# Performance work log

Hardware: AMD Instinct MI355X
Metric: run time of the kernel (lower is better)

Reference implementation:

```python
import jax, jax.numpy as jnp
import numpy as np

N_TOK, BATCH, D, MEM, H, W = 196, 64, 256, 2048, 16, 16


def setup_inputs() -> dict:
    key = jax.random.key(0)
    ks = jax.random.split(key, 9)
    w_scale = 1.0 / np.sqrt(D)  # ~ Linear default init scale
    return {
        "input_tokens": jax.random.normal(ks[0], (N_TOK, BATCH, D), jnp.float32),
        "ch_memory": jax.random.normal(ks[1], (MEM, D), jnp.float32) * 0.1,
        "ch_wq": jax.random.normal(ks[2], (D, D), jnp.float32) * w_scale,
        "ch_wk": jax.random.normal(ks[3], (D, D), jnp.float32) * w_scale,
        "ch_wv": jax.random.normal(ks[4], (D, D), jnp.float32) * w_scale,
        "sp_memory": jax.random.normal(ks[5], (MEM, H, W), jnp.float32) * 0.1,
        "sp_wq": jax.random.normal(ks[6], (D, D), jnp.float32) * w_scale,
        "sp_wk": jax.random.normal(ks[7], (D, D), jnp.float32) * w_scale,
        "sp_wv": jax.random.normal(ks[8], (D, D), jnp.float32) * w_scale,
    }


def reference(input_tokens, ch_memory, ch_wq, ch_wk, ch_wv,
              sp_memory, sp_wq, sp_wk, sp_wv):
    n_tok, batch, d = input_tokens.shape
    hw = d  # spatial branch requires feature_dim == H*W
    x = input_tokens.reshape(n_tok * batch, d)  # [NB, D]

    # ---- Channel memory branch: dot-product softmax read ----
    q = x @ ch_wq.T                       # [NB, D]
    k = ch_memory @ ch_wk.T               # [M, D]
    v = ch_memory @ ch_wv.T               # [M, D]
    scores = (q @ k.T) * (1.0 / jnp.sqrt(jnp.float32(d)))  # [NB, M]
    att_c = jax.nn.softmax(scores, axis=-1)
    out_c = att_c @ v                     # [NB, D]

    # ---- Spatial memory branch: SSIM-score softmax read ----
    mem_flat = sp_memory.reshape(sp_memory.shape[0], hw)  # [M, HW]
    qf = x @ sp_wq.T                      # [NB, HW]
    kf = mem_flat @ sp_wk.T               # [M, HW]
    vf = mem_flat @ sp_wv.T               # [M, HW]

    q_mean = jnp.mean(qf, axis=1, keepdims=True)          # [NB, 1]
    k_mean = jnp.mean(kf, axis=1, keepdims=True)          # [M, 1]
    q_var = jnp.var(qf, axis=1, ddof=1, keepdims=True)    # unbiased, like torch.var
    k_var = jnp.var(kf, axis=1, ddof=1, keepdims=True)
    cov = ((qf - q_mean) @ (kf - k_mean).T) / jnp.float32(hw - 1)  # [NB, M]

    c1, c2 = 0.01, 0.03
    mean_prod = q_mean @ k_mean.T                          # [NB, M]
    numerator = (2.0 * mean_prod + c1) * (2.0 * cov + c2)
    denominator = (q_mean ** 2 + (k_mean.T) ** 2 + c1) * (q_var + k_var.T + c2)
    ssim = numerator / (denominator + 1e-8)                # [NB, M]

    att_s = jax.nn.softmax(ssim, axis=-1)
    out_s = att_s @ vf                     # [NB, HW] == [NB, D]

    return (out_c + out_s).reshape(n_tok, batch, d)
```

## Files before the change

### kernel.cpp

```cpp
#include <hip/hip_runtime.h>

#define NBQ 12544
#define DM  256
#define MM  2048

typedef __attribute__((ext_vector_type(8)))  __bf16 bf16x8;
typedef __attribute__((ext_vector_type(4)))  float  floatx4;

__device__ __forceinline__ ushort f2bf(float x) {
    unsigned u = __float_as_uint(x);
    u += 0x7fffu + ((u >> 16) & 1u);
    return (ushort)(u >> 16);
}
__device__ __forceinline__ float bf2f(ushort h) {
    return __uint_as_float(((unsigned)h) << 16);
}

__device__ __forceinline__ void glds16(const ushort* g, ushort* l) {
    __builtin_amdgcn_global_load_lds(
        (const __attribute__((address_space(1))) unsigned int*)g,
        (__attribute__((address_space(3))) unsigned int*)l, 16, 0, 0);
}

__global__ __launch_bounds__(256) void gemm_proj_all(
    const float* __restrict__ x,      const float* __restrict__ ch_mem,
    const float* __restrict__ ch_wq,  const float* __restrict__ ch_wk,
    const float* __restrict__ ch_wv,  const float* __restrict__ sp_mem,
    const float* __restrict__ sp_wq,  const float* __restrict__ sp_wk,
    const float* __restrict__ sp_wv,
    ushort* __restrict__ Qb,  ushort* __restrict__ QFb,
    ushort* __restrict__ Kb,  ushort* __restrict__ KFb,
    ushort* __restrict__ Vtb, ushort* __restrict__ VFtb)
{
    __shared__ ushort As[64][72];
    __shared__ ushort W1s[64][72];
    __shared__ ushort W2s[64][72];

    int bid = blockIdx.x;
    const float* A; const float* W1; const float* W2;
    ushort* C1; ushort* C2; int nrows, trans2;
    if (bid < 784) {
        A = x; W1 = ch_wq; W2 = sp_wq; C1 = Qb; C2 = QFb; nrows = NBQ; trans2 = 0;
    } else if (bid < 912) {
        A = ch_mem; W1 = ch_wk; W2 = ch_wv; C1 = Kb; C2 = Vtb;
        nrows = MM; trans2 = 1; bid -= 784;
    } else {
        A = sp_mem; W1 = sp_wk; W2 = sp_wv; C1 = KFb; C2 = VFtb;
        nrows = MM; trans2 = 1; bid -= 912;
    }
    const int r0 = (bid >> 2) * 64;
    const int c0 = (bid & 3) * 64;

    const int tid  = threadIdx.x;
    const int wv   = tid >> 6;
    const int lane = tid & 63;
    const int quad = lane >> 4;
    const int l16  = lane & 15;
    const int rw = (wv & 1) * 32;
    const int cw = (wv >> 1) * 32;

    floatx4 acc1[2][2], acc2[2][2];
    #pragma unroll
    for (int i = 0; i < 2; ++i)
        #pragma unroll
        for (int j = 0; j < 2; ++j) {
            acc1[i][j] = (floatx4){0.f, 0.f, 0.f, 0.f};
            acc2[i][j] = (floatx4){0.f, 0.f, 0.f, 0.f};
        }

    for (int d0 = 0; d0 < 256; d0 += 64) {
        __syncthreads();
        #pragma unroll
        for (int it = 0; it < 4; ++it) {
            int idx = tid + it * 256;
            int r = idx >> 4, c4 = (idx & 15) * 4;
            float4 a4 = *(const float4*)(A  + (size_t)(r0 + r) * 256 + d0 + c4);
            float4 w14 = *(const float4*)(W1 + (size_t)(c0 + r) * 256 + d0 + c4);
            float4 w24 = *(const float4*)(W2 + (size_t)(c0 + r) * 256 + d0 + c4);
            ushort4 ab, w1b, w2b;
            ab.x = f2bf(a4.x);  ab.y = f2bf(a4.y);  ab.z = f2bf(a4.z);  ab.w = f2bf(a4.w);
            w1b.x = f2bf(w14.x); w1b.y = f2bf(w14.y); w1b.z = f2bf(w14.z); w1b.w = f2bf(w14.w);
            w2b.x = f2bf(w24.x); w2b.y = f2bf(w24.y); w2b.z = f2bf(w24.z); w2b.w = f2bf(w24.w);
            *(ushort4*)&As[r][c4]  = ab;
            *(ushort4*)&W1s[r][c4] = w1b;
            *(ushort4*)&W2s[r][c4] = w2b;
        }
        __syncthreads();
        #pragma unroll
        for (int kk = 0; kk < 64; kk += 32) {
            bf16x8 aA0 = *(const bf16x8*)&As[rw + l16][kk + quad * 8];
            bf16x8 aA1 = *(const bf16x8*)&As[rw + 16 + l16][kk + quad * 8];
            bf16x8 b10 = *(const bf16x8*)&W1s[cw + l16][kk + quad * 8];
            bf16x8 b11 = *(const bf16x8*)&W1s[cw + 16 + l16][kk + quad * 8];
            bf16x8 b20 = *(const bf16x8*)&W2s[cw + l16][kk + quad * 8];
            bf16x8 b21 = *(const bf16x8*)&W2s[cw + 16 + l16][kk + quad * 8];
            acc1[0][0] = __builtin_amdgcn_mfma_f32_16x16x32_bf16(aA0, b10, acc1[0][0], 0, 0, 0);
            acc1[0][1] = __builtin_amdgcn_mfma_f32_16x16x32_bf16(aA0, b11, acc1[0][1], 0, 0, 0);
            acc1[1][0] = __builtin_amdgcn_mfma_f32_16x16x32_bf16(aA1, b10, acc1[1][0], 0, 0, 0);
            acc1[1][1] = __builtin_amdgcn_mfma_f32_16x16x32_bf16(aA1, b11, acc1[1][1], 0, 0, 0);
            acc2[0][0] = __builtin_amdgcn_mfma_f32_16x16x32_bf16(aA0, b20, acc2[0][0], 0, 0, 0);
            acc2[0][1] = __builtin_amdgcn_mfma_f32_16x16x32_bf16(aA0, b21, acc2[0][1], 0, 0, 0);
            acc2[1][0] = __builtin_amdgcn_mfma_f32_16x16x32_bf16(aA1, b20, acc2[1][0], 0, 0, 0);
            acc2[1][1] = __builtin_amdgcn_mfma_f32_16x16x32_bf16(aA1, b21, acc2[1][1], 0, 0, 0);
        }
    }

    #pragma unroll
    for (int ag = 0; ag < 2; ++ag)
        #pragma unroll
        for (int cg = 0; cg < 2; ++cg)
            #pragma unroll
            for (int i = 0; i < 4; ++i)
                C1[(size_t)(r0 + rw + ag * 16 + quad * 4 + i) * 256
                   + c0 + cw + cg * 16 + l16] = f2bf(acc1[ag][cg][i]);

    if (!trans2) {
        #pragma unroll
        for (int ag = 0; ag < 2; ++ag)
            #pragma unroll
            for (int cg = 0; cg < 2; ++cg)
                #pragma unroll
                for (int i = 0; i < 4; ++i)
                    C2[(size_t)(r0 + rw + ag * 16 + quad * 4 + i) * 256
                       + c0 + cw + cg * 16 + l16] = f2bf(acc2[ag][cg][i]);
    } else {
        __syncthreads();
        #pragma unroll
        for (int ag = 0; ag < 2; ++ag)
            #pragma unroll
            for (int cg = 0; cg < 2; ++cg)
                #pragma unroll
                for (int i = 0; i < 4; ++i)
                    W2s[cw + cg * 16 + l16][rw + ag * 16 + quad * 4 + i] = f2bf(acc2[ag][cg][i]);
        __syncthreads();
        const int col = tid >> 2;
        const int seg = (tid & 3) * 16;
        #pragma unroll
        for (int j = 0; j < 2; ++j)
            *(uint4*)(C2 + (size_t)(c0 + col) * nrows + r0 + seg + j * 8) =
                *(const uint4*)&W2s[col][seg + j * 8];
    }
}

__global__ __launch_bounds__(256) void row_stats_kf(
    const ushort* __restrict__ KFb, float* __restrict__ km, float* __restrict__ kv)
{
    const int row  = blockIdx.x * 4 + (threadIdx.x >> 6);
    const int lane = threadIdx.x & 63;
    ushort4 u = *(const ushort4*)(KFb + (size_t)row * 256 + lane * 4);
    float a = bf2f(u.x), b = bf2f(u.y), c = bf2f(u.z), d = bf2f(u.w);
    float s  = a + b + c + d;
    float ss = a * a + b * b + c * c + d * d;
    #pragma unroll
    for (int off = 32; off > 0; off >>= 1) {
        s  += __shfl_down(s, off);
        ss += __shfl_down(ss, off);
    }
    if (lane == 0) {
        float m = s * (1.f / 256.f);
        km[row] = m;
        kv[row] = (ss - 256.f * m * m) * (1.f / 255.f);
    }
}

template<int NHALF>
__global__ __launch_bounds__(256, 2) void fused_attn_st(
    const ushort* __restrict__ Qb,  const ushort* __restrict__ QFb,
    const ushort* __restrict__ Kb,  const ushort* __restrict__ KFb,
    const ushort* __restrict__ Vtb, const ushort* __restrict__ VFtb,
    const float* __restrict__ km_, const float* __restrict__ kv_,
    float* __restrict__ out, float* __restrict__ part, float* __restrict__ denp)
{
    __shared__ ushort SMu[32768];
    float* combuf = (float*)SMu;

    const int tid  = threadIdx.x;
    const int wv   = tid >> 6;
    const int lane = tid & 63;
    const int quad = lane >> 4;
    const int l16  = lane & 15;
    const int qsel = wv & 1;
    const int br   = wv >> 1;

    const int bid   = blockIdx.x;
    const int half  = (NHALF == 2) ? (bid & 1) : 0;
    const int qc    = (NHALF == 2) ? (bid >> 1) : bid;
    const int q0    = qc * 32;
    const int kbase = half * (MM / NHALF);
    const int NT    = (MM / NHALF) / 32;

    const ushort* qsrc = br ? QFb : Qb;
    bf16x8 aQ[8];
    {
        const ushort* qp = qsrc + (size_t)(q0 + qsel * 16 + l16) * DM + quad * 8;
        #pragma unroll
        for (int s = 0; s < 8; ++s) aQ[s] = *(const bf16x8*)(qp + s * 32);
    }

    float qmv = 0.f, qvv = 0.f;
    if (br) {
        float sum = 0.f, ss = 0.f;
        #pragma unroll
        for (int s = 0; s < 8; ++s)
            #pragma unroll
            for (int j = 0; j < 8; ++j) {
                float v = (float)aQ[s][j];
                sum += v; ss += v * v;
            }
        sum += __shfl_xor(sum, 16, 64); sum += __shfl_xor(sum, 32, 64);
        ss  += __shfl_xor(ss, 16, 64);  ss  += __shfl_xor(ss, 32, 64);
        qmv = sum * (1.f / 256.f);
        qvv = (ss - 256.f * qmv * qmv) * (1.f / 255.f);
    }

    int offK[4], offV[4];
    #pragma unroll
    for (int p = 0; p < 4; ++p) {
        int j  = wv * 4 + p;
        int Rk = 2 * j + (lane >> 5);
        int rk = (Rk & 3) + ((Rk >> 4) & 1) * 4 + ((Rk >> 2) & 3) * 8;
        int ck = (lane & 31) ^ (Rk & 7);
        offK[p] = rk * DM + ck * 8;
        int Rv = 16 * j + (lane >> 2);
        int cv = (lane & 3) ^ (Rv & 3);
        offV[p] = Rv * MM + cv * 8;
    }

    const ushort* kp  = Kb   + (size_t)kbase * DM;
    const ushort* kfp = KFb  + (size_t)kbase * DM;
    const ushort* vp  = Vtb  + kbase;
    const ushort* vfp = VFtb + kbase;

    floatx4 acc[16];
    #pragma unroll
    for (int t = 0; t < 16; ++t) acc[t] = (floatx4){0.f, 0.f, 0.f, 0.f};
    float den = 0.f;

    const int ksw  = l16 & 7;
    const int vswo = (quad ^ (l16 & 3)) * 8;

    for (int ti = 0; ti < NT; ++ti) {
        __syncthreads();
        #pragma unroll
        for (int p = 0; p < 4; ++p) {
            int db = (wv * 4 + p) * 512;
            glds16(kp  + offK[p], SMu + db);
            glds16(kfp + offK[p], SMu + 8192 + db);
            glds16(vp  + offV[p], SMu + 16384 + db);
            glds16(vfp + offV[p], SMu + 24576 + db);
        }
        kp += 32 * DM; kfp += 32 * DM; vp += 32; vfp += 32;
        __syncthreads();

        const ushort* Ks = SMu + (br ? 8192 : 0);
        floatx4 S0 = (floatx4){0.f, 0.f, 0.f, 0.f};
        floatx4 S1 = (floatx4){0.f, 0.f, 0.f, 0.f};
        #pragma unroll
        for (int s = 0; s < 8; ++s) {
            int off = (((s * 4 + quad) ^ ksw)) * 8;
            bf16x8 aK0 = *(const bf16x8*)(Ks + l16 * DM + off);
            bf16x8 aK1 = *(const bf16x8*)(Ks + 4096 + l16 * DM + off);
            S0 = __builtin_amdgcn_mfma_f32_16x16x32_bf16(aK0, aQ[s], S0, 0, 0, 0);
            S1 = __builtin_amdgcn_mfma_f32_16x16x32_bf16(aK1, aQ[s], S1, 0, 0, 0);
        }

        const int kk = kbase + ti * 32;
        float pb[8];
        if (!br) {
            #pragma unroll
            for (int r = 0; r < 4; ++r) {
                pb[r]     = __expf(S0[r] * 0.0625f);
                pb[4 + r] = __expf(S1[r] * 0.0625f);
            }
        } else {
            floatx4 km0 = *(const floatx4*)(km_ + kk + 8 * quad);
            floatx4 km1 = *(const floatx4*)(km_ + kk + 8 * quad + 4);
            floatx4 kv0 = *(const floatx4*)(kv_ + kk + 8 * quad);
            floatx4 kv1 = *(const floatx4*)(kv_ + kk + 8 * quad + 4);
            #pragma unroll
            for (int r = 0; r < 4; ++r) {
                {
                    float mp  = qmv * km0[r];
                    float cov = (S0[r] - 256.f * mp) * (1.f / 255.f);
                    float num = (2.f * mp + 0.01f) * (2.f * cov + 0.03f);
                    float dn  = (qmv * qmv + km0[r] * km0[r] + 0.01f) * (qvv + kv0[r] + 0.03f);
                    pb[r] = __expf(num / (dn + 1e-8f));
                }
                {
                    float mp  = qmv * km1[r];
                    float cov = (S1[r] - 256.f * mp) * (1.f / 255.f);
                    float num = (2.f * mp + 0.01f) * (2.f * cov + 0.03f);
                    float dn  = (qmv * qmv + km1[r] * km1[r] + 0.01f) * (qvv + kv1[r] + 0.03f);
                    pb[4 + r] = __expf(num / (dn + 1e-8f));
                }
            }
        }
        union { ushort u[8]; bf16x8 v; } ap;
        #pragma unroll
        for (int j = 0; j < 8; ++j) {
            den += pb[j];
            ap.u[j] = f2bf(pb[j]);
        }

        const ushort* Vs = SMu + (br ? 24576 : 16384);
        #pragma unroll
        for (int t = 0; t < 16; ++t) {
            bf16x8 bV = *(const bf16x8*)(Vs + (t * 16 + l16) * 32 + vswo);
            acc[t] = __builtin_amdgcn_mfma_f32_16x16x32_bf16(ap.v, bV, acc[t], 0, 0, 0);
        }
    }

    den += __shfl_xor(den, 16, 64);
    den += __shfl_xor(den, 32, 64);

    if (NHALF == 1) {
        float rdn[4];
        #pragma unroll
        for (int r = 0; r < 4; ++r)
            rdn[r] = 1.f / __shfl(den, quad * 4 + r, 64);

        __syncthreads();
        if (br) {
            #pragma unroll
            for (int t = 0; t < 16; ++t)
                #pragma unroll
                for (int r = 0; r < 4; ++r)
                    combuf[(qsel * 16 + quad * 4 + r) * 256 + t * 16 + l16] = acc[t][r] * rdn[r];
        }
        __syncthreads();
        if (!br) {
            #pragma unroll
            for (int t = 0; t < 16; ++t)
                #pragma unroll
                for (int r = 0; r < 4; ++r) {
                    int ql = qsel * 16 + quad * 4 + r;
                    out[(size_t)(q0 + ql) * DM + t * 16 + l16] =
                        acc[t][r] * rdn[r] + combuf[ql * 256 + t * 16 + l16];
                }
        }
    } else {
        float* Np = part + (size_t)(half * 2 + br) * ((size_t)NBQ * DM);
        #pragma unroll
        for (int t = 0; t < 16; ++t)
            #pragma unroll
            for (int r = 0; r < 4; ++r)
                Np[(size_t)(q0 + qsel * 16 + quad * 4 + r) * DM + t * 16 + l16] = acc[t][r];
        if (lane < 16)
            denp[(size_t)(half * 2 + br) * NBQ + q0 + qsel * 16 + lane] = den;
    }
}

__global__ __launch_bounds__(256) void combine_halves(
    const float* __restrict__ part, const float* __restrict__ denp,
    float* __restrict__ out)
{
    const size_t stride = (size_t)NBQ * 64;
    const float4* p4 = (const float4*)part;
    float4* o4 = (float4*)out;
    #pragma unroll
    for (int u = 0; u < 2; ++u) {
        size_t i = (size_t)blockIdx.x * 512 + (size_t)u * 256 + threadIdx.x;
        int q = (int)(i >> 6);
        float rc = 1.f / (denp[q] + denp[2 * NBQ + q]);
        float rs = 1.f / (denp[NBQ + q] + denp[3 * NBQ + q]);
        float4 c0 = p4[i];
        float4 s0 = p4[stride + i];
        float4 c1 = p4[2 * stride + i];
        float4 s1 = p4[3 * stride + i];
        float4 r;
        r.x = (c0.x + c1.x) * rc + (s0.x + s1.x) * rs;
        r.y = (c0.y + c1.y) * rc + (s0.y + s1.y) * rs;
        r.z = (c0.z + c1.z) * rc + (s0.z + s1.z) * rs;
        r.w = (c0.w + c1.w) * rc + (s0.w + s1.w) * rs;
        o4[i] = r;
    }
}

extern "C" void kernel_launch(void* const* d_in, const int* in_sizes, int n_in,
                              void* d_out, int out_size, void* d_ws, size_t ws_size,
                              hipStream_t stream)
{
    const float* x      = (const float*)d_in[0];
    const float* ch_mem = (const float*)d_in[1];
    const float* ch_wq  = (const float*)d_in[2];
    const float* ch_wk  = (const float*)d_in[3];
    const float* ch_wv  = (const float*)d_in[4];
    const float* sp_mem = (const float*)d_in[5];
    const float* sp_wq  = (const float*)d_in[6];
    const float* sp_wk  = (const float*)d_in[7];
    const float* sp_wv  = (const float*)d_in[8];
    float* out = (float*)d_out;

    ushort* Qb   = (ushort*)d_ws;
    ushort* QFb  = Qb   + (size_t)NBQ * DM;
    ushort* Kb   = QFb  + (size_t)NBQ * DM;
    ushort* KFb  = Kb   + (size_t)MM * DM;
    ushort* Vtb  = KFb  + (size_t)MM * DM;
    ushort* VFtb = Vtb  + (size_t)MM * DM;
    float*  km   = (float*)(VFtb + (size_t)MM * DM);
    float*  kv   = km + MM;
    float*  part = kv + MM;
    float*  denp = part + (size_t)4 * NBQ * DM;

    const size_t base_b = (2 * (size_t)NBQ * DM + 4 * (size_t)MM * DM) * sizeof(ushort)
                        + 2 * (size_t)MM * sizeof(float);
    const size_t need   = base_b + ((size_t)4 * NBQ * DM + 4 * NBQ) * sizeof(float);
    const bool split = ws_size >= need;

    dim3 blk(256);
    gemm_proj_all<<<dim3(1040), blk, 0, stream>>>(
        x, ch_mem, ch_wq, ch_wk, ch_wv, sp_mem, sp_wq, sp_wk, sp_wv,
        Qb, QFb, Kb, KFb, Vtb, VFtb);
    row_stats_kf<<<dim3(MM / 4), blk, 0, stream>>>(KFb, km, kv);
    if (split) {
        fused_attn_st<2><<<dim3(2 * NBQ / 32), blk, 0, stream>>>(
            Qb, QFb, Kb, KFb, Vtb, VFtb, km, kv, out, part, denp);
        combine_halves<<<dim3(NBQ * DM / 4 / 512), blk, 0, stream>>>(part, denp, out);
    } else {
        fused_attn_st<1><<<dim3(NBQ / 32), blk, 0, stream>>>(
            Qb, QFb, Kb, KFb, Vtb, VFtb, km, kv, out, part, denp);
    }
}
```

Measured before the change: 287.9 us.

## Read K/V tiles directly from global memory instead of staging through LDS

The attention kernel stops cooperatively staging K, KF, V and VF tiles into shared memory with global_load_lds and barriers. Each wave now loads its MFMA operands straight from global memory (relying on L1/L2 caching), and LDS shrinks to the combine buffer. With less LDS in use, the launch bound is raised to three blocks per SM. This removes the two barriers per tile and the LDS traffic, but it risks uncoalesced, redundant global loads and exposed load latency without explicit prefetching.

After: 603.7 us. 110% more time.

```diff
diff --git a/kernel.cpp b/kernel.cpp
--- a/kernel.cpp
+++ b/kernel.cpp
@@ -14,12 +14,6 @@
 }
 __device__ __forceinline__ float bf2f(ushort h) {
     return __uint_as_float(((unsigned)h) << 16);
-}
-
-__device__ __forceinline__ void glds16(const ushort* g, ushort* l) {
-    __builtin_amdgcn_global_load_lds(
-        (const __attribute__((address_space(1))) unsigned int*)g,
-        (__attribute__((address_space(3))) unsigned int*)l, 16, 0, 0);
 }
 
 __global__ __launch_bounds__(256) void gemm_proj_all(
@@ -164,15 +158,14 @@
 }
 
 template<int NHALF>
-__global__ __launch_bounds__(256, 2) void fused_attn_st(
+__global__ __launch_bounds__(256, 3) void fused_attn_st(
     const ushort* __restrict__ Qb,  const ushort* __restrict__ QFb,
     const ushort* __restrict__ Kb,  const ushort* __restrict__ KFb,
     const ushort* __restrict__ Vtb, const ushort* __restrict__ VFtb,
     const float* __restrict__ km_, const float* __restrict__ kv_,
     float* __restrict__ out, float* __restrict__ part, float* __restrict__ denp)
 {
-    __shared__ ushort SMu[32768];
-    float* combuf = (float*)SMu;
+    __shared__ float combuf[(NHALF == 1) ? 8192 : 4];
 
     const int tid  = threadIdx.x;
     const int wv   = tid >> 6;
@@ -213,53 +206,25 @@
         qvv = (ss - 256.f * qmv * qmv) * (1.f / 255.f);
     }
 
-    int offK[4], offV[4];
-    #pragma unroll
-    for (int p = 0; p < 4; ++p) {
-        int j  = wv * 4 + p;
-        int Rk = 2 * j + (lane >> 5);
-        int rk = (Rk & 3) + ((Rk >> 4) & 1) * 4 + ((Rk >> 2) & 3) * 8;
-        int ck = (lane & 31) ^ (Rk & 7);
-        offK[p] = rk * DM + ck * 8;
-        int Rv = 16 * j + (lane >> 2);
-        int cv = (lane & 3) ^ (Rv & 3);
-        offV[p] = Rv * MM + cv * 8;
-    }
-
-    const ushort* kp  = Kb   + (size_t)kbase * DM;
-    const ushort* kfp = KFb  + (size_t)kbase * DM;
-    const ushort* vp  = Vtb  + kbase;
-    const ushort* vfp = VFtb + kbase;
+    const ushort* Ksel = br ? KFb : Kb;
+    const ushort* Vsel = br ? VFtb : Vtb;
+    const int rk0 = (l16 & 3) + (l16 >> 2) * 8;
+    const ushort* kp0 = Ksel + (size_t)(kbase + rk0) * DM + quad * 8;
+    const ushort* kp1 = kp0 + 4 * DM;
+    const ushort* vp  = Vsel + (size_t)l16 * MM + kbase + quad * 8;
 
     floatx4 acc[16];
     #pragma unroll
     for (int t = 0; t < 16; ++t) acc[t] = (floatx4){0.f, 0.f, 0.f, 0.f};
     float den = 0.f;
 
-    const int ksw  = l16 & 7;
-    const int vswo = (quad ^ (l16 & 3)) * 8;
-
     for (int ti = 0; ti < NT; ++ti) {
-        __syncthreads();
-        #pragma unroll
-        for (int p = 0; p < 4; ++p) {
-            int db = (wv * 4 + p) * 512;
-            glds16(kp  + offK[p], SMu + db);
-            glds16(kfp + offK[p], SMu + 8192 + db);
-            glds16(vp  + offV[p], SMu + 16384 + db);
-            glds16(vfp + offV[p], SMu + 24576 + db);
-        }
-        kp += 32 * DM; kfp += 32 * DM; vp += 32; vfp += 32;
-        __syncthreads();
-
-        const ushort* Ks = SMu + (br ? 8192 : 0);
         floatx4 S0 = (floatx4){0.f, 0.f, 0.f, 0.f};
         floatx4 S1 = (floatx4){0.f, 0.f, 0.f, 0.f};
         #pragma unroll
         for (int s = 0; s < 8; ++s) {
-            int off = (((s * 4 + quad) ^ ksw)) * 8;
-            bf16x8 aK0 = *(const bf16x8*)(Ks + l16 * DM + off);
-            bf16x8 aK1 = *(const bf16x8*)(Ks + 4096 + l16 * DM + off);
+            bf16x8 aK0 = *(const bf16x8*)(kp0 + s * 32);
+            bf16x8 aK1 = *(const bf16x8*)(kp1 + s * 32);
             S0 = __builtin_amdgcn_mfma_f32_16x16x32_bf16(aK0, aQ[s], S0, 0, 0, 0);
             S1 = __builtin_amdgcn_mfma_f32_16x16x32_bf16(aK1, aQ[s], S1, 0, 0, 0);
         }
@@ -302,12 +267,15 @@
             ap.u[j] = f2bf(pb[j]);
         }
 
-        const ushort* Vs = SMu + (br ? 24576 : 16384);
         #pragma unroll
         for (int t = 0; t < 16; ++t) {
-            bf16x8 bV = *(const bf16x8*)(Vs + (t * 16 + l16) * 32 + vswo);
+            bf16x8 bV = *(const bf16x8*)(vp + (size_t)t * 16 * MM);
             acc[t] = __builtin_amdgcn_mfma_f32_16x16x32_bf16(ap.v, bV, acc[t], 0, 0, 0);
         }
+
+        kp0 += 32 * DM;
+        kp1 += 32 * DM;
+        vp  += 32;
     }
 
     den += __shfl_xor(den, 16, 64);
```

## Split attention by branch, enlarge query tile, double-buffer K/V, prefetch projection loads

Applied to the files above, without the earlier changes.

The attention kernel now handles one branch per block, with each wave owning 32 queries (128 per block). Each K/V tile in shared memory is therefore reused across more queries, and only one branch's K and V is loaded. K/V tiles are double-buffered so the next tile's global-to-LDS load overlaps the current tile's MFMA work, and the key range is split four ways when workspace allows, with partial results reduced in a generalised combine kernel. The projection GEMM also prefetches the next k-slice into registers. The cost is higher register pressure (two accumulator sets of 16 floatx4), a larger partial-sum workspace (8 slices instead of 4), and more combine traffic.

After: 258.2 us. -10.3%, faster.

```diff
diff --git a/kernel.cpp b/kernel.cpp
--- a/kernel.cpp
+++ b/kernel.cpp
@@ -68,22 +68,39 @@
             acc2[i][j] = (floatx4){0.f, 0.f, 0.f, 0.f};
         }
 
+    float4 a4[4], w14[4], w24[4];
+    #pragma unroll
+    for (int it = 0; it < 4; ++it) {
+        int idx = tid + it * 256;
+        int r = idx >> 4, c4 = (idx & 15) * 4;
+        a4[it]  = *(const float4*)(A  + (size_t)(r0 + r) * 256 + c4);
+        w14[it] = *(const float4*)(W1 + (size_t)(c0 + r) * 256 + c4);
+        w24[it] = *(const float4*)(W2 + (size_t)(c0 + r) * 256 + c4);
+    }
+
     for (int d0 = 0; d0 < 256; d0 += 64) {
         __syncthreads();
         #pragma unroll
         for (int it = 0; it < 4; ++it) {
             int idx = tid + it * 256;
             int r = idx >> 4, c4 = (idx & 15) * 4;
-            float4 a4 = *(const float4*)(A  + (size_t)(r0 + r) * 256 + d0 + c4);
-            float4 w14 = *(const float4*)(W1 + (size_t)(c0 + r) * 256 + d0 + c4);
-            float4 w24 = *(const float4*)(W2 + (size_t)(c0 + r) * 256 + d0 + c4);
             ushort4 ab, w1b, w2b;
-            ab.x = f2bf(a4.x);  ab.y = f2bf(a4.y);  ab.z = f2bf(a4.z);  ab.w = f2bf(a4.w);
-            w1b.x = f2bf(w14.x); w1b.y = f2bf(w14.y); w1b.z = f2bf(w14.z); w1b.w = f2bf(w14.w);
-            w2b.x = f2bf(w24.x); w2b.y = f2bf(w24.y); w2b.z = f2bf(w24.z); w2b.w = f2bf(w24.w);
+            ab.x = f2bf(a4[it].x);  ab.y = f2bf(a4[it].y);  ab.z = f2bf(a4[it].z);  ab.w = f2bf(a4[it].w);
+            w1b.x = f2bf(w14[it].x); w1b.y = f2bf(w14[it].y); w1b.z = f2bf(w14[it].z); w1b.w = f2bf(w14[it].w);
+            w2b.x = f2bf(w24[it].x); w2b.y = f2bf(w24[it].y); w2b.z = f2bf(w24[it].z); w2b.w = f2bf(w24[it].w);
             *(ushort4*)&As[r][c4]  = ab;
             *(ushort4*)&W1s[r][c4] = w1b;
             *(ushort4*)&W2s[r][c4] = w2b;
+        }
+        if (d0 + 64 < 256) {
+            #pragma unroll
+            for (int it = 0; it < 4; ++it) {
+                int idx = tid + it * 256;
+                int r = idx >> 4, c4 = (idx & 15) * 4;
+                a4[it]  = *(const float4*)(A  + (size_t)(r0 + r) * 256 + d0 + 64 + c4);
+                w14[it] = *(const float4*)(W1 + (size_t)(c0 + r) * 256 + d0 + 64 + c4);
+                w24[it] = *(const float4*)(W2 + (size_t)(c0 + r) * 256 + d0 + 64 + c4);
+            }
         }
         __syncthreads();
         #pragma unroll
@@ -163,54 +180,78 @@
     }
 }
 
+#define STAGE_TILE(b, ti)                                                     \
+    {                                                                         \
+        const ushort* kp_ = kp0 + (size_t)(ti) * 32 * DM;                     \
+        const ushort* vp_ = vp0 + (ti) * 32;                                  \
+        ushort* dst_ = SMu + (b) * 16384;                                     \
+        _Pragma("unroll")                                                     \
+        for (int p = 0; p < 4; ++p) {                                         \
+            int db = (wv * 4 + p) * 512;                                      \
+            glds16(kp_ + offK[p], dst_ + db);                                 \
+            glds16(vp_ + offV[p], dst_ + 8192 + db);                          \
+        }                                                                     \
+    }
+
 template<int NHALF>
-__global__ __launch_bounds__(256, 2) void fused_attn_st(
+__global__ __launch_bounds__(256, 2) void fused_attn_1br(
     const ushort* __restrict__ Qb,  const ushort* __restrict__ QFb,
     const ushort* __restrict__ Kb,  const ushort* __restrict__ KFb,
     const ushort* __restrict__ Vtb, const ushort* __restrict__ VFtb,
     const float* __restrict__ km_, const float* __restrict__ kv_,
-    float* __restrict__ out, float* __restrict__ part, float* __restrict__ denp)
+    float* __restrict__ part, float* __restrict__ denp)
 {
     __shared__ ushort SMu[32768];
-    float* combuf = (float*)SMu;
 
     const int tid  = threadIdx.x;
     const int wv   = tid >> 6;
     const int lane = tid & 63;
     const int quad = lane >> 4;
     const int l16  = lane & 15;
-    const int qsel = wv & 1;
-    const int br   = wv >> 1;
-
-    const int bid   = blockIdx.x;
-    const int half  = (NHALF == 2) ? (bid & 1) : 0;
-    const int qc    = (NHALF == 2) ? (bid >> 1) : bid;
-    const int q0    = qc * 32;
+
+    const int NQC = NBQ / 128;
+    const int per_br = NQC * NHALF;
+    int bid = blockIdx.x;
+    const int br  = (bid < per_br) ? 1 : 0;
+    int rem = br ? bid : bid - per_br;
+    const int half = rem / NQC;
+    const int qc   = rem - half * NQC;
+    const int q0   = qc * 128;
     const int kbase = half * (MM / NHALF);
-    const int NT    = (MM / NHALF) / 32;
+    const int NT   = (MM / NHALF) / 32;
 
     const ushort* qsrc = br ? QFb : Qb;
-    bf16x8 aQ[8];
+    const ushort* Ksel = br ? KFb : Kb;
+    const ushort* Vsel = br ? VFtb : Vtb;
+
+    bf16x8 aQ0[8], aQ1[8];
     {
-        const ushort* qp = qsrc + (size_t)(q0 + qsel * 16 + l16) * DM + quad * 8;
-        #pragma unroll
-        for (int s = 0; s < 8; ++s) aQ[s] = *(const bf16x8*)(qp + s * 32);
-    }
-
-    float qmv = 0.f, qvv = 0.f;
+        const ushort* qp = qsrc + (size_t)(q0 + wv * 32 + l16) * DM + quad * 8;
+        #pragma unroll
+        for (int s = 0; s < 8; ++s) {
+            aQ0[s] = *(const bf16x8*)(qp + s * 32);
+            aQ1[s] = *(const bf16x8*)(qp + 16 * DM + s * 32);
+        }
+    }
+
+    float qmv0 = 0.f, qvv0 = 0.f, qmv1 = 0.f, qvv1 = 0.f;
     if (br) {
-        float sum = 0.f, ss = 0.f;
+        float s0 = 0.f, ss0 = 0.f, s1 = 0.f, ss1 = 0.f;
         #pragma unroll
         for (int s = 0; s < 8; ++s)
             #pragma unroll
             for (int j = 0; j < 8; ++j) {
-                float v = (float)aQ[s][j];
-                sum += v; ss += v * v;
-            }
-        sum += __shfl_xor(sum, 16, 64); sum += __shfl_xor(sum, 32, 64);
-        ss  += __shfl_xor(ss, 16, 64);  ss  += __shfl_xor(ss, 32, 64);
-        qmv = sum * (1.f / 256.f);
-        qvv = (ss - 256.f * qmv * qmv) * (1.f / 255.f);
+                float v0 = (float)aQ0[s][j], v1 = (float)aQ1[s][j];
+                s0 += v0; ss0 += v0 * v0; s1 += v1; ss1 += v1 * v1;
+            }
+        s0  += __shfl_xor(s0, 16, 64);  s0  += __shfl_xor(s0, 32, 64);
+        ss0 += __shfl_xor(ss0, 16, 64); ss0 += __shfl_xor(ss0, 32, 64);
+        s1  += __shfl_xor(s1, 16, 64);  s1  += __shfl_xor(s1, 32, 64);
+        ss1 += __shfl_xor(ss1, 16, 64); ss1 += __shfl_xor(ss1, 32, 64);
+        qmv0 = s0 * (1.f / 256.f);
+        qvv0 = (ss0 - 256.f * qmv0 * qmv0) * (1.f / 255.f);
+        qmv1 = s1 * (1.f / 256.f);
+        qvv1 = (ss1 - 256.f * qmv1 * qmv1) * (1.f / 255.f);
     }
 
     int offK[4], offV[4];
@@ -226,57 +267,234 @@
         offV[p] = Rv * MM + cv * 8;
     }
 
-    const ushort* kp  = Kb   + (size_t)kbase * DM;
-    const ushort* kfp = KFb  + (size_t)kbase * DM;
-    const ushort* vp  = Vtb  + kbase;
-    const ushort* vfp = VFtb + kbase;
-
-    floatx4 acc[16];
-    #pragma unroll
-    for (int t = 0; t < 16; ++t) acc[t] = (floatx4){0.f, 0.f, 0.f, 0.f};
-    float den = 0.f;
-
+    const ushort* kp0 = Ksel + (size_t)kbase * DM;
+    const ushort* vp0 = Vsel + kbase;
+
+    floatx4 acc0[16], acc1[16];
+    #pragma unroll
+    for (int t = 0; t < 16; ++t) {
+        acc0[t] = (floatx4){0.f, 0.f, 0.f, 0.f};
+        acc1[t] = (floatx4){0.f, 0.f, 0.f, 0.f};
+    }
+    float den0 = 0.f, den1 = 0.f;
     const int ksw  = l16 & 7;
     const int vswo = (quad ^ (l16 & 3)) * 8;
 
+    STAGE_TILE(0, 0);
+    __syncthreads();
+
+    int buf = 0;
     for (int ti = 0; ti < NT; ++ti) {
-        __syncthreads();
-        #pragma unroll
-        for (int p = 0; p < 4; ++p) {
-            int db = (wv * 4 + p) * 512;
-            glds16(kp  + offK[p], SMu + db);
-            glds16(kfp + offK[p], SMu + 8192 + db);
-            glds16(vp  + offV[p], SMu + 16384 + db);
-            glds16(vfp + offV[p], SMu + 24576 + db);
-        }
-        kp += 32 * DM; kfp += 32 * DM; vp += 32; vfp += 32;
-        __syncthreads();
-
-        const ushort* Ks = SMu + (br ? 8192 : 0);
-        floatx4 S0 = (floatx4){0.f, 0.f, 0.f, 0.f};
-        floatx4 S1 = (floatx4){0.f, 0.f, 0.f, 0.f};
+        if (ti + 1 < NT) STAGE_TILE(buf ^ 1, ti + 1);
+
+        const ushort* Ks = SMu + buf * 16384;
+        const ushort* Vs = Ks + 8192;
+
+        floatx4 S00 = (floatx4){0.f, 0.f, 0.f, 0.f};
+        floatx4 S10 = (floatx4){0.f, 0.f, 0.f, 0.f};
+        floatx4 S01 = (floatx4){0.f, 0.f, 0.f, 0.f};
+        floatx4 S11 = (floatx4){0.f, 0.f, 0.f, 0.f};
         #pragma unroll
         for (int s = 0; s < 8; ++s) {
-            int off = (((s * 4 + quad) ^ ksw)) * 8;
+            int off = ((s * 4 + quad) ^ ksw) * 8;
             bf16x8 aK0 = *(const bf16x8*)(Ks + l16 * DM + off);
             bf16x8 aK1 = *(const bf16x8*)(Ks + 4096 + l16 * DM + off);
-            S0 = __builtin_amdgcn_mfma_f32_16x16x32_bf16(aK0, aQ[s], S0, 0, 0, 0);
-            S1 = __builtin_amdgcn_mfma_f32_16x16x32_bf16(aK1, aQ[s], S1, 0, 0, 0);
+            S00 = __builtin_amdgcn_mfma_f32_16x16x32_bf16(aK0, aQ0[s], S00, 0, 0, 0);
+            S10 = __builtin_amdgcn_mfma_f32_16x16x32_bf16(aK1, aQ0[s], S10, 0, 0, 0);
+            S01 = __builtin_amdgcn_mfma_f32_16x16x32_bf16(aK0, aQ1[s], S01, 0, 0, 0);
+            S11 = __builtin_amdgcn_mfma_f32_16x16x32_bf16(aK1, aQ1[s], S11, 0, 0, 0);
         }
 
         const int kk = kbase + ti * 32;
-        float pb[8];
+        float p0[8], p1[8];
         if (!br) {
             #pragma unroll
             for (int r = 0; r < 4; ++r) {
-                pb[r]     = __expf(S0[r] * 0.0625f);
-                pb[4 + r] = __expf(S1[r] * 0.0625f);
+                p0[r]     = __expf(S00[r] * 0.0625f);
+                p0[4 + r] = __expf(S10[r] * 0.0625f);
+                p1[r]     = __expf(S01[r] * 0.0625f);
+                p1[4 + r] = __expf(S11[r] * 0.0625f);
             }
         } else {
             floatx4 km0 = *(const floatx4*)(km_ + kk + 8 * quad);
             floatx4 km1 = *(const floatx4*)(km_ + kk + 8 * quad + 4);
             floatx4 kv0 = *(const floatx4*)(kv_ + kk + 8 * quad);
             floatx4 kv1 = *(const floatx4*)(kv_ + kk + 8 * quad + 4);
+            #pragma unroll
+            for (int r = 0; r < 4; ++r) {
+                {
+                    float mp  = qmv0 * km0[r];
+                    float cov = (S00[r] - 256.f * mp) * (1.f / 255.f);
+                    float num = (2.f * mp + 0.01f) * (2.f * cov + 0.03f);
+                    float dn  = (qmv0 * qmv0 + km0[r] * km0[r] + 0.01f) * (qvv0 + kv0[r] + 0.03f);
+                    p0[r] = __expf(num / (dn + 1e-8f));
+                }
+                {
+                    float mp  = qmv0 * km1[r];
+                    float cov = (S10[r] - 256.f * mp) * (1.f / 255.f);
+                    float num = (2.f * mp + 0.01f) * (2.f * cov + 0.03f);
+                    float dn  = (qmv0 * qmv0 + km1[r] * km1[r] + 0.01f) * (qvv0 + kv1[r] + 0.03f);
+                    p0[4 + r] = __expf(num / (dn + 1e-8f));
+                }
+                {
+                    float mp  = qmv1 * km0[r];
+                    float cov = (S01[r] - 256.f * mp) * (1.f / 255.f);
+                    float num = (2.f * mp + 0.01f) * (2.f * cov + 0.03f);
+                    float dn  = (qmv1 * qmv1 + km0[r] * km0[r] + 0.01f) * (qvv1 + kv0[r] + 0.03f);
+                    p1[r] = __expf(num / (dn + 1e-8f));
+                }
+                {
+                    float mp  = qmv1 * km1[r];
+                    float cov = (S11[r] - 256.f * mp) * (1.f / 255.f);
+                    float num = (2.f * mp + 0.01f) * (2.f * cov + 0.03f);
+                    float dn  = (qmv1 * qmv1 + km1[r] * km1[r] + 0.01f) * (qvv1 + kv1[r] + 0.03f);
+                    p1[4 + r] = __expf(num / (dn + 1e-8f));
+                }
+            }
+        }
+        union { ushort u[8]; bf16x8 v; } ap0, ap1;
+        #pragma unroll
+        for (int j = 0; j < 8; ++j) {
+            den0 += p0[j]; ap0.u[j] = f2bf(p0[j]);
+            den1 += p1[j]; ap1.u[j] = f2bf(p1[j]);
+        }
+
+        #pragma unroll
+        for (int t = 0; t < 16; ++t) {
+            bf16x8 bV = *(const bf16x8*)(Vs + (t * 16 + l16) * 32 + vswo);
+            acc0[t] = __builtin_amdgcn_mfma_f32_16x16x32_bf16(ap0.v, bV, acc0[t], 0, 0, 0);
+            acc1[t] = __builtin_amdgcn_mfma_f32_16x16x32_bf16(ap1.v, bV, acc1[t], 0, 0, 0);
+        }
+
+        __syncthreads();
+        buf ^= 1;
+    }
+
+    den0 += __shfl_xor(den0, 16, 64); den0 += __shfl_xor(den0, 32, 64);
+    den1 += __shfl_xor(den1, 16, 64); den1 += __shfl_xor(den1, 32, 64);
+
+    const int sec = br * NHALF + half;
+    float* Np = part + (size_t)sec * ((size_t)NBQ * DM);
+    #pragma unroll
+    for (int t = 0; t < 16; ++t)
+        #pragma unroll
+        for (int r = 0; r < 4; ++r) {
+            int row = q0 + wv * 32 + quad * 4 + r;
+            Np[(size_t)row * DM + t * 16 + l16]        = acc0[t][r];
+            Np[(size_t)(row + 16) * DM + t * 16 + l16] = acc1[t][r];
+        }
+    if (lane < 16) {
+        denp[(size_t)sec * NBQ + q0 + wv * 32 + lane]      = den0;
+        denp[(size_t)sec * NBQ + q0 + wv * 32 + 16 + lane] = den1;
+    }
+}
+
+__global__ __launch_bounds__(256, 2) void fused_attn_fb(
+    const ushort* __restrict__ Qb,  const ushort* __restrict__ QFb,
+    const ushort* __restrict__ Kb,  const ushort* __restrict__ KFb,
+    const ushort* __restrict__ Vtb, const ushort* __restrict__ VFtb,
+    const float* __restrict__ km_, const float* __restrict__ kv_,
+    float* __restrict__ out)
+{
+    __shared__ ushort SMu[32768];
+    float* combuf = (float*)SMu;
+
+    const int tid  = threadIdx.x;
+    const int wv   = tid >> 6;
+    const int lane = tid & 63;
+    const int quad = lane >> 4;
+    const int l16  = lane & 15;
+    const int qsel = wv & 1;
+    const int br   = wv >> 1;
+    const int q0   = blockIdx.x * 32;
+
+    const ushort* qsrc = br ? QFb : Qb;
+    bf16x8 aQ[8];
+    {
+        const ushort* qp = qsrc + (size_t)(q0 + qsel * 16 + l16) * DM + quad * 8;
+        #pragma unroll
+        for (int s = 0; s < 8; ++s) aQ[s] = *(const bf16x8*)(qp + s * 32);
+    }
+
+    float qmv = 0.f, qvv = 0.f;
+    if (br) {
+        float sum = 0.f, ss = 0.f;
+        #pragma unroll
+        for (int s = 0; s < 8; ++s)
+            #pragma unroll
+            for (int j = 0; j < 8; ++j) {
+                float v = (float)aQ[s][j];
+                sum += v; ss += v * v;
+            }
+        sum += __shfl_xor(sum, 16, 64); sum += __shfl_xor(sum, 32, 64);
+        ss  += __shfl_xor(ss, 16, 64);  ss  += __shfl_xor(ss, 32, 64);
+        qmv = sum * (1.f / 256.f);
+        qvv = (ss - 256.f * qmv * qmv) * (1.f / 255.f);
+    }
+
+    int offK[4], offV[4];
+    #pragma unroll
+    for (int p = 0; p < 4; ++p) {
+        int j  = wv * 4 + p;
+        int Rk = 2 * j + (lane >> 5);
+        int rk = (Rk & 3) + ((Rk >> 4) & 1) * 4 + ((Rk >> 2) & 3) * 8;
+        int ck = (lane & 31) ^ (Rk & 7);
+        offK[p] = rk * DM + ck * 8;
+        int Rv = 16 * j + (lane >> 2);
+        int cv = (lane & 3) ^ (Rv & 3);
+        offV[p] = Rv * MM + cv * 8;
+    }
+
+    const ushort* kp  = Kb;
+    const ushort* kfp = KFb;
+    const ushort* vp  = Vtb;
+    const ushort* vfp = VFtb;
+
+    floatx4 acc[16];
+    #pragma unroll
+    for (int t = 0; t < 16; ++t) acc[t] = (floatx4){0.f, 0.f, 0.f, 0.f};
+    float den = 0.f;
+
+    const int ksw  = l16 & 7;
+    const int vswo = (quad ^ (l16 & 3)) * 8;
+
+    for (int kt = 0; kt < MM; kt += 32) {
+        __syncthreads();
+        #pragma unroll
+        for (int p = 0; p < 4; ++p) {
+            int db = (wv * 4 + p) * 512;
+            glds16(kp  + offK[p], SMu + db);
+            glds16(kfp + offK[p], SMu + 4096 + db);
+            glds16(vp  + offV[p], SMu + 16384 + db);
+            glds16(vfp + offV[p], SMu + 24576 + db);
+        }
+        kp += 32 * DM; kfp += 32 * DM; vp += 32; vfp += 32;
+        __syncthreads();
+
+        const ushort* Ks = SMu + (br ? 4096 : 0);
+        floatx4 S0 = (floatx4){0.f, 0.f, 0.f, 0.f};
+        floatx4 S1 = (floatx4){0.f, 0.f, 0.f, 0.f};
+        #pragma unroll
+        for (int s = 0; s < 8; ++s) {
+            int off = ((s * 4 + quad) ^ ksw) * 8;
+            bf16x8 aK0 = *(const bf16x8*)(Ks + l16 * DM + off);
+            bf16x8 aK1 = *(const bf16x8*)(Ks + 2048 + l16 * DM + off);
+            S0 = __builtin_amdgcn_mfma_f32_16x16x32_bf16(aK0, aQ[s], S0, 0, 0, 0);
+            S1 = __builtin_amdgcn_mfma_f32_16x16x32_bf16(aK1, aQ[s], S1, 0, 0, 0);
+        }
+
+        float pb[8];
+        if (!br) {
+            #pragma unroll
+            for (int r = 0; r < 4; ++r) {
+                pb[r]     = __expf(S0[r] * 0.0625f);
+                pb[4 + r] = __expf(S1[r] * 0.0625f);
+            }
+        } else {
+            floatx4 km0 = *(const floatx4*)(km_ + kt + 8 * quad);
+            floatx4 km1 = *(const floatx4*)(km_ + kt + 8 * quad + 4);
+            floatx4 kv0 = *(const floatx4*)(kv_ + kt + 8 * quad);
+            floatx4 kv1 = *(const floatx4*)(kv_ + kt + 8 * quad + 4);
             #pragma unroll
             for (int r = 0; r < 4; ++r) {
                 {
@@ -312,44 +530,33 @@
 
     den += __shfl_xor(den, 16, 64);
     den += __shfl_xor(den, 32, 64);
-
-    if (NHALF == 1) {
-        float rdn[4];
-        #pragma unroll
-        for (int r = 0; r < 4; ++r)
-            rdn[r] = 1.f / __shfl(den, quad * 4 + r, 64);
-
-        __syncthreads();
-        if (br) {
-            #pragma unroll
-            for (int t = 0; t < 16; ++t)
-                #pragma unroll
-                for (int r = 0; r < 4; ++r)
-                    combuf[(qsel * 16 + quad * 4 + r) * 256 + t * 16 + l16] = acc[t][r] * rdn[r];
-        }
-        __syncthreads();
-        if (!br) {
-            #pragma unroll
-            for (int t = 0; t < 16; ++t)
-                #pragma unroll
-                for (int r = 0; r < 4; ++r) {
-                    int ql = qsel * 16 + quad * 4 + r;
-                    out[(size_t)(q0 + ql) * DM + t * 16 + l16] =
-                        acc[t][r] * rdn[r] + combuf[ql * 256 + t * 16 + l16];
-                }
-        }
-    } else {
-        float* Np = part + (size_t)(half * 2 + br) * ((size_t)NBQ * DM);
+    float rdn[4];
+    #pragma unroll
+    for (int r = 0; r < 4; ++r)
+        rdn[r] = 1.f / __shfl(den, quad * 4 + r, 64);
+
+    __syncthreads();
+    if (br) {
         #pragma unroll
         for (int t = 0; t < 16; ++t)
             #pragma unroll
             for (int r = 0; r < 4; ++r)
-                Np[(size_t)(q0 + qsel * 16 + quad * 4 + r) * DM + t * 16 + l16] = acc[t][r];
-        if (lane < 16)
-            denp[(size_t)(half * 2 + br) * NBQ + q0 + qsel * 16 + lane] = den;
-    }
-}
-
+                combuf[(qsel * 16 + quad * 4 + r) * 256 + t * 16 + l16] = acc[t][r] * rdn[r];
+    }
+    __syncthreads();
+    if (!br) {
+        #pragma unroll
+        for (int t = 0; t < 16; ++t)
+            #pragma unroll
+            for (int r = 0; r < 4; ++r) {
+                int ql = qsel * 16 + quad * 4 + r;
+                out[(size_t)(q0 + ql) * DM + t * 16 + l16] =
+                    acc[t][r] * rdn[r] + combuf[ql * 256 + t * 16 + l16];
+            }
+    }
+}
+
+template<int NH>
 __global__ __launch_bounds__(256) void combine_halves(
     const float* __restrict__ part, const float* __restrict__ denp,
     float* __restrict__ out)
@@ -361,17 +568,26 @@
     for (int u = 0; u < 2; ++u) {
         size_t i = (size_t)blockIdx.x * 512 + (size_t)u * 256 + threadIdx.x;
         int q = (int)(i >> 6);
-        float rc = 1.f / (denp[q] + denp[2 * NBQ + q]);
-        float rs = 1.f / (denp[NBQ + q] + denp[3 * NBQ + q]);
-        float4 c0 = p4[i];
-        float4 s0 = p4[stride + i];
-        float4 c1 = p4[2 * stride + i];
-        float4 s1 = p4[3 * stride + i];
+        float dc = 0.f, ds = 0.f;
+        #pragma unroll
+        for (int h = 0; h < NH; ++h) {
+            dc += denp[(size_t)h * NBQ + q];
+            ds += denp[(size_t)(NH + h) * NBQ + q];
+        }
+        float rc = 1.f / dc, rs = 1.f / ds;
+        float4 nc = {0.f, 0.f, 0.f, 0.f}, ns = {0.f, 0.f, 0.f, 0.f};
+        #pragma unroll
+        for (int h = 0; h < NH; ++h) {
+            float4 c = p4[(size_t)h * stride + i];
+            float4 s = p4[(size_t)(NH + h) * stride + i];
+            nc.x += c.x; nc.y += c.y; nc.z += c.z; nc.w += c.w;
+            ns.x += s.x; ns.y += s.y; ns.z += s.z; ns.w += s.w;
+        }
         float4 r;
-        r.x = (c0.x + c1.x) * rc + (s0.x + s1.x) * rs;
-        r.y = (c0.y + c1.y) * rc + (s0.y + s1.y) * rs;
-        r.z = (c0.z + c1.z) * rc + (s0.z + s1.z) * rs;
-        r.w = (c0.w + c1.w) * rc + (s0.w + s1.w) * rs;
+        r.x = nc.x * rc + ns.x * rs;
+        r.y = nc.y * rc + ns.y * rs;
+        r.z = nc.z * rc + ns.z * rs;
+        r.w = nc.w * rc + ns.w * rs;
         o4[i] = r;
     }
 }
@@ -399,25 +615,28 @@
     ushort* VFtb = Vtb  + (size_t)MM * DM;
     float*  km   = (float*)(VFtb + (size_t)MM * DM);
     float*  kv   = km + MM;
-    float*  part = kv + MM;
-    float*  denp = part + (size_t)4 * NBQ * DM;
-
-    const size_t base_b = (2 * (size_t)NBQ * DM + 4 * (size_t)MM * DM) * sizeof(ushort)
-                        + 2 * (size_t)MM * sizeof(float);
-    const size_t need   = base_b + ((size_t)4 * NBQ * DM + 4 * NBQ) * sizeof(float);
-    const bool split = ws_size >= need;
+    float*  denp = kv + MM;
+    float*  part = denp + (size_t)8 * NBQ;
+
+    const size_t base_b = (size_t)((char*)part - (char*)d_ws);
+    const size_t need4  = base_b + (size_t)8 * NBQ * DM * sizeof(float);
+    const size_t need2  = base_b + (size_t)4 * NBQ * DM * sizeof(float);
 
     dim3 blk(256);
     gemm_proj_all<<<dim3(1040), blk, 0, stream>>>(
         x, ch_mem, ch_wq, ch_wk, ch_wv, sp_mem, sp_wq, sp_wk, sp_wv,
         Qb, QFb, Kb, KFb, Vtb, VFtb);
     row_stats_kf<<<dim3(MM / 4), blk, 0, stream>>>(KFb, km, kv);
-    if (split) {
-        fused_attn_st<2><<<dim3(2 * NBQ / 32), blk, 0, stream>>>(
-            Qb, QFb, Kb, KFb, Vtb, VFtb, km, kv, out, part, denp);
-        combine_halves<<<dim3(NBQ * DM / 4 / 512), blk, 0, stream>>>(part, denp, out);
+    if (ws_size >= need4) {
+        fused_attn_1br<4><<<dim3(2 * (NBQ / 128) * 4), blk, 0, stream>>>(
+            Qb, QFb, Kb, KFb, Vtb, VFtb, km, kv, part, denp);
+        combine_halves<4><<<dim3(NBQ * DM / 4 / 512), blk, 0, stream>>>(part, denp, out);
+    } else if (ws_size >= need2) {
+        fused_attn_1br<2><<<dim3(2 * (NBQ / 128) * 2), blk, 0, stream>>>(
+            Qb, QFb, Kb, KFb, Vtb, VFtb, km, kv, part, denp);
+        combine_halves<2><<<dim3(NBQ * DM / 4 / 512), blk, 0, stream>>>(part, denp, out);
     } else {
-        fused_attn_st<1><<<dim3(NBQ / 32), blk, 0, stream>>>(
-            Qb, QFb, Kb, KFb, Vtb, VFtb, km, kv, out, part, denp);
-    }
-}
+        fused_attn_fb<<<dim3(NBQ / 32), blk, 0, stream>>>(
+            Qb, QFb, Kb, KFb, Vtb, VFtb, km, kv, out);
+    }
+}
```
